# Kernel optimization log

Hardware: AMD Instinct MI355X
Metric: run time of the kernel (lower is better)

The kernel has to match this reference:

```python
import jax, jax.numpy as jnp
import numpy as np

N_NODES = 50000
N_EDGES = 800000
C = 64
N_STEPS = 4
N_MIX = 14  # sum_{i=0..3} (i+2)
NEG_SLOPE = 0.2  # PyG GATConv default negative_slope


def setup_inputs() -> dict:
    key = jax.random.key(0)
    ks = jax.random.split(key, 9)
    g = lambda k, shp: jax.random.normal(k, shp, jnp.float32) * (1.0 / np.sqrt(C))
    return {
        "x": jax.random.normal(ks[0], (N_NODES, C), jnp.float32),
        "edge_index": jax.random.randint(ks[1], (2, N_EDGES), 0, N_NODES, dtype=jnp.int64),
        "alphas": jax.random.normal(ks[2], (N_MIX, 5), jnp.float32),
        "gcn_W": g(ks[3], (N_MIX, C, C)),
        "gcn_b": jnp.zeros((N_MIX, C), jnp.float32),
        "sage_Wl": g(ks[4], (N_MIX, C, C)),
        "sage_Wr": g(ks[5], (N_MIX, C, C)),
        "sage_b": jnp.zeros((N_MIX, C), jnp.float32),
        "gat_W": g(ks[6], (N_MIX, C, C)),
        "gat_a_src": g(ks[7], (N_MIX, C)),
        "gat_a_dst": g(ks[8], (N_MIX, C)),
        "gat_b": jnp.zeros((N_MIX, C), jnp.float32),
    }


def _cell(x, edge_index, alphas, gcn_W, gcn_b, sage_Wl, sage_Wr, sage_b,
          gat_W, gat_a_src, gat_a_dst, gat_b):
    n = x.shape[0]
    src, dst = edge_index[0], edge_index[1]
    loop = jnp.arange(n)
    # edges with self-loops (used by GCN and GAT, per PyG defaults)
    src_sl = jnp.concatenate([src, loop])
    dst_sl = jnp.concatenate([dst, loop])

    # GCN symmetric normalization: deg over self-looped targets, norm per edge.
    deg = jax.ops.segment_sum(jnp.ones(src_sl.shape, jnp.float32), dst_sl, num_segments=n)
    dinv = jnp.where(deg > 0, jax.lax.rsqrt(deg), 0.0)
    gcn_norm = dinv[src_sl] * dinv[dst_sl]  # [E+N]

    # SAGE mean-aggregation denominator (no self loops; empty -> clamp to 1, sum is 0 anyway)
    cnt = jnp.maximum(
        jax.ops.segment_sum(jnp.ones(dst.shape, jnp.float32), dst, num_segments=n), 1.0)

    def gcn(h, k):
        hw = h @ gcn_W[k]  # [n, C]
        return jax.ops.segment_sum(gcn_norm[:, None] * hw[src_sl], dst_sl,
                                   num_segments=n) + gcn_b[k]

    def sage(h, k):
        agg = jax.ops.segment_sum(h[src], dst, num_segments=n) / cnt[:, None]
        return agg @ sage_Wl[k] + h @ sage_Wr[k] + sage_b[k]

    def gat(h, k):
        hw = h @ gat_W[k]  # shared lin for src/dst (same node set)
        e = (hw @ gat_a_src[k])[src_sl] + (hw @ gat_a_dst[k])[dst_sl]
        e = jnp.where(e > 0, e, NEG_SLOPE * e)  # LeakyReLU
        # segment softmax over incoming edges per target (self-loops make all segments non-empty)
        emax = jax.ops.segment_max(e, dst_sl, num_segments=n)
        ee = jnp.exp(e - emax[dst_sl])
        denom = jax.ops.segment_sum(ee, dst_sl, num_segments=n)
        a = ee / denom[dst_sl]
        return jax.ops.segment_sum(a[:, None] * hw[src_sl], dst_sl,
                                   num_segments=n) + gat_b[k]

    def mixed(h, k):
        w = jax.nn.softmax(alphas[k])  # [5]: gcn, sage, gat, identity, zero
        return w[0] * gcn(h, k) + w[1] * sage(h, k) + w[2] * gat(h, k) + w[3] * h

    states = [x, x]
    offset = 0
    for i in range(N_STEPS):
        s = 0.0
        for j in range(i + 2):
            s = s + mixed(states[j], offset + j)
        offset += i + 2
        states.append(s)
    return jnp.mean(jnp.stack(states[-N_STEPS:], axis=0), axis=0)


def reference(x, edge_index, alphas, gcn_W, gcn_b, sage_Wl, sage_Wr, sage_b,
              gat_W, gat_a_src, gat_a_dst, gat_b):
    return _cell(x, edge_index, alphas, gcn_W, gcn_b, sage_Wl, sage_Wr, sage_b,
                 gat_W, gat_a_src, gat_a_dst, gat_b)
```

## Files before the change

### kernel.cpp

```cpp
#include <hip/hip_runtime.h>

#define N_NODES 50000
#define N_EDGES 800000
#define CCH 64
#define N_MIX 14
#define NBUCK 196
#define BCAP 6144
#define ECHUNK 3125

typedef __bf16 bf16x8 __attribute__((ext_vector_type(8)));
typedef float floatx4 __attribute__((ext_vector_type(4)));

__device__ __forceinline__ float leaky(float x) {
    return fmaxf(x, 0.2f * x);
}

__global__ void prep_weights(const float* __restrict__ alphas,
                             const float* __restrict__ gcn_W, const float* __restrict__ gcn_b,
                             const float* __restrict__ sage_Wl, const float* __restrict__ sage_Wr,
                             const float* __restrict__ sage_b, const float* __restrict__ gat_Wp,
                             const float* __restrict__ a_src, const float* __restrict__ a_dst,
                             const float* __restrict__ gat_b,
                             __bf16* __restrict__ Wt, float* __restrict__ bc,
                             float* __restrict__ vs, float* __restrict__ vd) {
    int k = blockIdx.x;
    __shared__ float w[5];
    if (threadIdx.x == 0) {
        float a[5], m = -1e30f, s = 0.f;
        for (int i = 0; i < 5; ++i) { a[i] = alphas[k * 5 + i]; m = fmaxf(m, a[i]); }
        for (int i = 0; i < 5; ++i) { a[i] = __expf(a[i] - m); s += a[i]; }
        for (int i = 0; i < 5; ++i) w[i] = a[i] / s;
    }
    __syncthreads();
    float gamma = (k >= 9) ? 0.25f : 1.0f;
    float w0 = gamma * w[0], w1 = gamma * w[1], w2 = gamma * w[2], w3 = gamma * w[3];
    float idext = (k >= 11) ? 0.25f : 0.f;
    for (int idx = threadIdx.x; idx < 64 * 256; idx += blockDim.x) {
        int c = idx >> 8, j = idx & 255;
        float v;
        if (j < 64)       v = w0 * gcn_W[k * 4096 + j * 64 + c];
        else if (j < 128) v = w1 * sage_Wl[k * 4096 + (j - 64) * 64 + c];
        else if (j < 192) {
            int jj = j - 128;
            v = w1 * sage_Wr[k * 4096 + jj * 64 + c];
            if (jj == c) v += w3 + idext;
        } else {
            v = w2 * gat_Wp[k * 4096 + (j - 192) * 64 + c];
        }
        Wt[(size_t)k * 16384 + idx] = (__bf16)v;
    }
    if (threadIdx.x < 64) {
        int r = threadIdx.x;
        bc[k * 64 + r] = gamma * (w[0] * gcn_b[k * 64 + r] + w[1] * sage_b[k * 64 + r] +
                                  w[2] * gat_b[k * 64 + r]);
        float s1 = 0.f, s2 = 0.f;
        for (int j = 0; j < 64; ++j) {
            float wv_ = gat_Wp[k * 4096 + r * 64 + j];
            s1 += wv_ * a_src[k * 64 + j];
            s2 += wv_ * a_dst[k * 64 + j];
        }
        vs[k * 64 + r] = s1;
        vd[k * 64 + r] = s2;
    }
}

__global__ void prep_scoreV(const float* __restrict__ vs, const float* __restrict__ vd,
                            __bf16* __restrict__ Vph,
                            unsigned km0, unsigned km1, unsigned km2, unsigned km3,
                            unsigned nks) {
    int p = blockIdx.x;
    unsigned km = (p == 0) ? km0 : (p == 1) ? km1 : (p == 2) ? km2 : km3;
    int nk = (nks >> (p * 4)) & 15;
    for (int idx = threadIdx.x; idx < 1024; idx += blockDim.x) {
        int n = idx >> 6, kk = idx & 63;
        int t = n & 7;
        float v = 0.f;
        if (t < nk) {
            int k = (km >> (4 * t)) & 15;
            v = (n < 8) ? vs[k * 64 + kk] : vd[k * 64 + kk];
        }
        Vph[p * 1024 + n * 64 + kk] = (__bf16)v;
    }
}

__global__ void convert_bf16(const float4* __restrict__ src, __bf16* __restrict__ dst, int n4) {
    int i = blockIdx.x * blockDim.x + threadIdx.x;
    if (i < n4) {
        float4 v = src[i];
        dst[i * 4 + 0] = (__bf16)v.x;
        dst[i * 4 + 1] = (__bf16)v.y;
        dst[i * 4 + 2] = (__bf16)v.z;
        dst[i * 4 + 3] = (__bf16)v.w;
    }
}

__global__ __launch_bounds__(256) void bucket_count(const int* __restrict__ ei,
                                                    int* __restrict__ bcount) {
    __shared__ int h[NBUCK];
    for (int i = threadIdx.x; i < NBUCK; i += 256) h[i] = 0;
    __syncthreads();
    int e0 = blockIdx.x * ECHUNK;
    for (int i = threadIdx.x; i < ECHUNK; i += 256)
        atomicAdd(&h[ei[N_EDGES + e0 + i] >> 8], 1);
    __syncthreads();
    for (int i = threadIdx.x; i < NBUCK; i += 256)
        if (h[i]) atomicAdd(&bcount[i], h[i]);
}

__global__ __launch_bounds__(256) void bucket_scan(const int* __restrict__ bcount,
                                                   int* __restrict__ bbase,
                                                   int* __restrict__ row_ptr) {
    __shared__ int s[256];
    int t = threadIdx.x;
    int v = (t < NBUCK) ? bcount[t] : 0;
    s[t] = v;
    __syncthreads();
    for (int o = 1; o < 256; o <<= 1) {
        int t2 = (t >= o) ? s[t - o] : 0;
        __syncthreads();
        s[t] += t2;
        __syncthreads();
    }
    if (t < NBUCK) bbase[t + 1] = s[t];
    if (t == 0) { bbase[0] = 0; row_ptr[N_NODES] = N_EDGES; }
}

__global__ __launch_bounds__(256) void bucket_scatter(const int* __restrict__ ei,
                                                      const int* __restrict__ bbase,
                                                      int* __restrict__ bfill,
                                                      unsigned* __restrict__ pairs) {
    __shared__ int lh[NBUCK], lbase[NBUCK], lcur[NBUCK];
    int tid = threadIdx.x;
    int e0 = blockIdx.x * ECHUNK;
    for (int i = tid; i < NBUCK; i += 256) { lh[i] = 0; lcur[i] = 0; }
    __syncthreads();
    for (int i = tid; i < ECHUNK; i += 256)
        atomicAdd(&lh[ei[N_EDGES + e0 + i] >> 8], 1);
    __syncthreads();
    for (int i = tid; i < NBUCK; i += 256)
        lbase[i] = bbase[i] + ((lh[i] > 0) ? atomicAdd(&bfill[i], lh[i]) : 0);
    __syncthreads();
    for (int i = tid; i < ECHUNK; i += 256) {
        int s = ei[e0 + i];
        int d = ei[N_EDGES + e0 + i];
        int b = d >> 8;
        int pos = atomicAdd(&lcur[b], 1);
        pairs[lbase[b] + pos] = (unsigned)s | ((unsigned)(d & 255) << 16);
    }
}

__global__ __launch_bounds__(256) void bucket_sort(const unsigned* __restrict__ pairs,
                                                   const int* __restrict__ bbase,
                                                   int* __restrict__ row_ptr,
                                                   int* __restrict__ col_idx,
                                                   float* __restrict__ dinv,
                                                   float* __restrict__ cntf) {
    int b = blockIdx.x;
    __shared__ unsigned buf[BCAP];
    __shared__ int hist[256], off[256], cur[256];
    int tid = threadIdx.x;
    hist[tid] = 0;
    __syncthreads();
    int base = bbase[b], cnt = bbase[b + 1] - base;
    if (cnt > BCAP) cnt = BCAP;
    for (int i = tid; i < cnt; i += 256) {
        unsigned pr = pairs[(size_t)base + i];
        buf[i] = pr;
        atomicAdd(&hist[(pr >> 16) & 255], 1);
    }
    __syncthreads();
    int v = hist[tid];
    off[tid] = v;
    __syncthreads();
    for (int o = 1; o < 256; o <<= 1) {
        int t2 = (tid >= o) ? off[tid - o] : 0;
        __syncthreads();
        off[tid] += t2;
        __syncthreads();
    }
    int excl = off[tid] - v;
    int node = b * 256 + tid;
    if (node < N_NODES) {
        row_ptr[node] = base + excl;
        dinv[node] = rsqrtf((float)(v + 1));
        cntf[node] = (float)(v > 0 ? v : 1);
    }
    cur[tid] = excl;
    __syncthreads();
    for (int i = tid; i < cnt; i += 256) {
        unsigned pr = buf[i];
        int ln = (pr >> 16) & 255;
        int pos = atomicAdd(&cur[ln], 1);
        col_idx[base + pos] = (int)(pr & 0xffffu);
    }
}

__global__ __launch_bounds__(256) void score_mfma(const __bf16* __restrict__ hb,
                                                  const __bf16* __restrict__ V,
                                                  float* __restrict__ ssrcS,
                                                  float* __restrict__ sdstS) {
    int tid = threadIdx.x;
    int wave = tid >> 6, lane = tid & 63;
    int quad = lane >> 4, mr = lane & 15;
    int r0 = blockIdx.x * 128 + wave * 32;
    bf16x8 b0 = *(const bf16x8*)(V + mr * 64 + (quad << 3));
    bf16x8 b1 = *(const bf16x8*)(V + mr * 64 + 32 + (quad << 3));
#pragma unroll
    for (int rt = 0; rt < 2; ++rt) {
        int r = r0 + rt * 16 + mr;
        if (r > N_NODES - 1) r = N_NODES - 1;
        bf16x8 a0 = *(const bf16x8*)(hb + (size_t)r * 64 + (quad << 3));
        bf16x8 a1 = *(const bf16x8*)(hb + (size_t)r * 64 + 32 + (quad << 3));
        floatx4 acc = (floatx4){0.f, 0.f, 0.f, 0.f};
        acc = __builtin_amdgcn_mfma_f32_16x16x32_bf16(a0, b0, acc, 0, 0, 0);
        acc = __builtin_amdgcn_mfma_f32_16x16x32_bf16(a1, b1, acc, 0, 0, 0);
#pragma unroll
        for (int reg = 0; reg < 4; ++reg) {
            int row = r0 + rt * 16 + quad * 4 + reg;
            if (row < N_NODES) {
                if (mr < 8) ssrcS[(size_t)row * 8 + mr] = acc[reg];
                else        sdstS[(size_t)row * 8 + (mr - 8)] = acc[reg];
            }
        }
    }
}

template <int NK>
__global__ __launch_bounds__(128, 4) void fused_gather(
    const __bf16* __restrict__ hb, const int* __restrict__ row_ptr,
    const int* __restrict__ col_idx, const float* __restrict__ dinv,
    const float* __restrict__ cntf, const float* __restrict__ ssrcS,
    const float* __restrict__ sdstS, int soff, int doGS,
    __bf16* __restrict__ aggG, __bf16* __restrict__ aggS, __bf16* __restrict__ A) {
    int wid = blockIdx.x * 2 + (threadIdx.x >> 6);
    int lane = threadIdx.x & 63;
    int sub = lane >> 3, ln = lane & 7;
    int node = wid * 8 + sub;
    int beg = row_ptr[node], end = row_ptr[node + 1];

    float sd[NK], selfraw[NK];
    {
        float4 sv = *(const float4*)(ssrcS + (size_t)node * 8 + soff);
        float4 dvv = *(const float4*)(sdstS + (size_t)node * 8 + soff);
        float svv[4] = {sv.x, sv.y, sv.z, sv.w};
        float dvl[4] = {dvv.x, dvv.y, dvv.z, dvv.w};
#pragma unroll
        for (int t = 0; t < NK; ++t) {
            sd[t] = dvl[t];
            selfraw[t] = leaky(svv[t] + sd[t]);
        }
    }
    bf16x8 hsb = *(const bf16x8*)(hb + (size_t)node * 64 + ln * 8);
    float hs[8];
#pragma unroll
    for (int c = 0; c < 8; ++c) hs[c] = (float)hsb[c];

    float denoml[NK], acc[NK][8], accG[8], accS[8];
#pragma unroll
    for (int c = 0; c < 8; ++c) { accG[c] = 0.f; accS[c] = 0.f; }
#pragma unroll
    for (int t = 0; t < NK; ++t) {
        denoml[t] = 0.f;
#pragma unroll
        for (int c = 0; c < 8; ++c) acc[t][c] = hs[c];
    }
    for (int base = beg; base < end; base += 8) {
        int e = base + ln;
        int col = 0;
        float dv = 0.f, wv[NK];
#pragma unroll
        for (int t = 0; t < NK; ++t) wv[t] = 0.f;
        if (e < end) {
            col = col_idx[e];
            dv = dinv[col];
            float4 sv = *(const float4*)(ssrcS + (size_t)col * 8 + soff);
            float svv[4] = {sv.x, sv.y, sv.z, sv.w};
#pragma unroll
            for (int t = 0; t < NK; ++t) {
                wv[t] = __expf(leaky(svv[t] + sd[t]) - selfraw[t]);
                denoml[t] += wv[t];
            }
        }
        int jcnt = end - base;
        if (jcnt > 8) jcnt = 8;
        int cs0 = __shfl(col, (sub << 3), 64);
        bf16x8 hx = *(const bf16x8*)(hb + (size_t)cs0 * 64 + ln * 8);
        for (int j = 0; j < jcnt; ++j) {
            bf16x8 hxn;
            if (j + 1 < jcnt) {
                int csn = __shfl(col, (sub << 3) | (j + 1), 64);
                hxn = *(const bf16x8*)(hb + (size_t)csn * 64 + ln * 8);
            }
            int srcl = (sub << 3) | j;
            float dvj = __shfl(dv, srcl, 64);
            float wj[NK];
#pragma unroll
            for (int t = 0; t < NK; ++t) wj[t] = __shfl(wv[t], srcl, 64);
#pragma unroll
            for (int c = 0; c < 8; ++c) {
                float f = (float)hx[c];
                accS[c] += f;
                accG[c] += dvj * f;
#pragma unroll
                for (int t = 0; t < NK; ++t) acc[t][c] += wj[t] * f;
            }
            hx = hxn;
        }
    }
    float denom[NK];
#pragma unroll
    for (int t = 0; t < NK; ++t) {
        float w = denoml[t];
#pragma unroll
        for (int off = 1; off < 8; off <<= 1) w += __shfl_xor(w, off, 64);
        denom[t] = w + 1.0f;
    }

    if (doGS) {
        float dvn = dinv[node];
        float cin = 1.0f / cntf[node];
        bf16x8 og, os;
#pragma unroll
        for (int c = 0; c < 8; ++c) {
            os[c] = (__bf16)(accS[c] * cin);
            og[c] = (__bf16)(dvn * accG[c] + dvn * dvn * hs[c]);
        }
        *(bf16x8*)(aggS + (size_t)node * 64 + ln * 8) = os;
        *(bf16x8*)(aggG + (size_t)node * 64 + ln * 8) = og;
    }
#pragma unroll
    for (int t = 0; t < NK; ++t) {
        bf16x8 oa;
        float inv = 1.0f / denom[t];
#pragma unroll
        for (int c = 0; c < 8; ++c) oa[c] = (__bf16)(acc[t][c] * inv);
        *(bf16x8*)(A + (size_t)t * N_NODES * 64 + (size_t)node * 64 + ln * 8) = oa;
    }
}

struct GArgs {
    const __bf16* G;
    const __bf16* S;
    const __bf16* Hb;
    const __bf16* A0;
    const __bf16* Wt;
    const float* bc;
    float* tg[4];
    __bf16* shadow_ptr;
    long long slot;
    int nk;
    int initmask;
    int shadow_t;
    int kidx[8];
    int tsel[8];
};

__global__ __launch_bounds__(256) void gemm_group(GArgs a) {
    __shared__ __bf16 Wl[64 * 264];
    int tid = threadIdx.x;
    int wave = tid >> 6, lane = tid & 63;
    int quad = lane >> 4, mr = lane & 15;
    int r0 = blockIdx.x * 128 + wave * 32;
    bf16x8 gf[2][2], sf[2][2], hf[2][2];
#pragma unroll
    for (int rt = 0; rt < 2; ++rt) {
        int r = r0 + rt * 16 + mr;
        if (r > N_NODES - 1) r = N_NODES - 1;
#pragma unroll
        for (int hh = 0; hh < 2; ++hh) {
            int colj = hh * 32 + (quad << 3);
            gf[rt][hh] = *(const bf16x8*)(a.G + (size_t)r * 64 + colj);
            sf[rt][hh] = *(const bf16x8*)(a.S + (size_t)r * 64 + colj);
            hf[rt][hh] = *(const bf16x8*)(a.Hb + (size_t)r * 64 + colj);
        }
    }
    floatx4 acc[2][4];
    float bsum[4];
#pragma unroll
    for (int rt = 0; rt < 2; ++rt)
#pragma unroll
        for (int ct = 0; ct < 4; ++ct) acc[rt][ct] = (floatx4){0.f, 0.f, 0.f, 0.f};
#pragma unroll
    for (int ct = 0; ct < 4; ++ct) bsum[ct] = 0.f;
    int runstart = 0;
    for (int t = 0; t < a.nk; ++t) {
        int k = a.kidx[t];
        __syncthreads();
        {
            const uint4* src = (const uint4*)(a.Wt + (size_t)k * 16384);
            for (int i = tid; i < 2048; i += 256) {
                int row = i >> 5, colj = (i & 31) << 3;
                *(uint4*)&Wl[row * 264 + colj] = src[i];
            }
        }
        __syncthreads();
        const __bf16* Ap = a.A0 + (size_t)t * a.slot;
        bf16x8 af[2][2];
#pragma unroll
        for (int rt = 0; rt < 2; ++rt) {
            int r = r0 + rt * 16 + mr;
            if (r > N_NODES - 1) r = N_NODES - 1;
#pragma unroll
            for (int hh = 0; hh < 2; ++hh)
                af[rt][hh] = *(const bf16x8*)(Ap + (size_t)r * 64 + hh * 32 + (quad << 3));
        }
        const float* bp = a.bc + k * 64;
#pragma unroll
        for (int ct = 0; ct < 4; ++ct) bsum[ct] += bp[ct * 16 + mr];
#pragma unroll
        for (int seg = 0; seg < 4; ++seg) {
#pragma unroll
            for (int hh = 0; hh < 2; ++hh) {
                int kt = seg * 2 + hh;
                bf16x8 a0 = (seg == 0) ? gf[0][hh] : (seg == 1) ? sf[0][hh]
                            : (seg == 2) ? hf[0][hh] : af[0][hh];
                bf16x8 a1 = (seg == 0) ? gf[1][hh] : (seg == 1) ? sf[1][hh]
                            : (seg == 2) ? hf[1][hh] : af[1][hh];
#pragma unroll
                for (int ct = 0; ct < 4; ++ct) {
                    bf16x8 bfr = *(const bf16x8*)&Wl[(ct * 16 + mr) * 264 + (kt << 5) + (quad << 3)];
                    acc[0][ct] = __builtin_amdgcn_mfma_f32_16x16x32_bf16(a0, bfr, acc[0][ct], 0, 0, 0);
                    acc[1][ct] = __builtin_amdgcn_mfma_f32_16x16x32_bf16(a1, bfr, acc[1][ct], 0, 0, 0);
                }
            }
        }
        bool flush = (t == a.nk - 1) || (a.tsel[t + 1] != a.tsel[t]);
        if (flush) {
            float* tgt = a.tg[a.tsel[t]];
            int init = (a.initmask >> runstart) & 1;
            bool shadow = (t == a.shadow_t);
            __bf16* sh = a.shadow_ptr;
#pragma unroll
            for (int rt = 0; rt < 2; ++rt) {
#pragma unroll
                for (int reg = 0; reg < 4; ++reg) {
                    int r = r0 + rt * 16 + quad * 4 + reg;
                    if (r < N_NODES) {
#pragma unroll
                        for (int ct = 0; ct < 4; ++ct) {
                            int c = ct * 16 + mr;
                            float v = acc[rt][ct][reg] + bsum[ct];
                            size_t idx = (size_t)r * 64 + c;
                            float nv = init ? v : (tgt[idx] + v);
                            tgt[idx] = nv;
                            if (shadow) sh[idx] = (__bf16)nv;
                        }
                    }
                }
            }
#pragma unroll
            for (int rt = 0; rt < 2; ++rt)
#pragma unroll
                for (int ct = 0; ct < 4; ++ct) acc[rt][ct] = (floatx4){0.f, 0.f, 0.f, 0.f};
#pragma unroll
            for (int ct = 0; ct < 4; ++ct) bsum[ct] = 0.f;
            runstart = t + 1;
        }
    }
}

extern "C" void kernel_launch(void* const* d_in, const int* in_sizes, int n_in,
                              void* d_out, int out_size, void* d_ws, size_t ws_size,
                              hipStream_t stream) {
    const float* x       = (const float*)d_in[0];
    const int*   ei      = (const int*)d_in[1];
    const float* alphas  = (const float*)d_in[2];
    const float* gcn_W   = (const float*)d_in[3];
    const float* gcn_b   = (const float*)d_in[4];
    const float* sage_Wl = (const float*)d_in[5];
    const float* sage_Wr = (const float*)d_in[6];
    const float* sage_b  = (const float*)d_in[7];
    const float* gat_W   = (const float*)d_in[8];
    const float* a_src   = (const float*)d_in[9];
    const float* a_dst   = (const float*)d_in[10];
    const float* gat_b   = (const float*)d_in[11];
    float* out = (float*)d_out;

    char* p = (char*)d_ws;
    auto alloc = [&](size_t bytes) -> char* {
        char* r = p;
        p += (bytes + 255) & ~(size_t)255;
        return r;
    };
    const size_t NCf = (size_t)N_NODES * CCH;
    const size_t NC32 = NCf * 4;
    const size_t NC16 = NCf * 2;
    float* sb[3];
    sb[0] = (float*)alloc(NC32);
    sb[1] = (float*)alloc(NC32);
    sb[2] = (float*)alloc(NC32);
    __bf16* hbuf[4];
    for (int i = 0; i < 4; ++i) hbuf[i] = (__bf16*)alloc(NC16);
    __bf16* aggG = (__bf16*)alloc(NC16);
    __bf16* aggS = (__bf16*)alloc(NC16);
    float* ssrcS = (float*)alloc((size_t)N_NODES * 8 * 4);
    float* sdstS = (float*)alloc((size_t)N_NODES * 8 * 4);
    float* dinv  = (float*)alloc(N_NODES * 4);
    float* cntf  = (float*)alloc(N_NODES * 4);
    int* row_ptr = (int*)alloc((N_NODES + 1) * 4);
    int* col_idx = (int*)alloc((size_t)N_EDGES * 4);
    unsigned* pairs = (unsigned*)alloc((size_t)N_EDGES * 4);
    int* bcount  = (int*)alloc(NBUCK * 4);
    int* bfill   = (int*)alloc(NBUCK * 4);
    int* bbase   = (int*)alloc((NBUCK + 1) * 4);
    __bf16* Wt   = (__bf16*)alloc((size_t)N_MIX * 16384 * 2);
    float* bcv   = (float*)alloc(N_MIX * 64 * 4);
    float* vs    = (float*)alloc(N_MIX * 64 * 4);
    float* vd    = (float*)alloc(N_MIX * 64 * 4);
    __bf16* Vph  = (__bf16*)alloc(4 * 1024 * 2);

    size_t used = (size_t)(p - (char*)d_ws);
    int navail = (int)((ws_size > used) ? ((ws_size - used) / NC16) : 0);
    if (navail < 1) navail = 1;
    if (navail > 8) navail = 8;
    __bf16* Abuf = (__bf16*)alloc((size_t)navail * NC16);

    hipMemsetAsync(bcount, 0, NBUCK * 4, stream);
    hipMemsetAsync(bfill, 0, NBUCK * 4, stream);

    prep_weights<<<N_MIX, 256, 0, stream>>>(alphas, gcn_W, gcn_b, sage_Wl, sage_Wr, sage_b,
                                            gat_W, a_src, a_dst, gat_b, Wt, bcv, vs, vd);
    prep_scoreV<<<4, 256, 0, stream>>>(vs, vd, Vph, 0xA9653210u, 0xB74u, 0xC8u, 0xDu, 0x1238u);
    convert_bf16<<<(int)((NCf / 4 + 255) / 256), 256, 0, stream>>>((const float4*)x, hbuf[0],
                                                                   (int)(NCf / 4));
    bucket_count<<<256, 256, 0, stream>>>(ei, bcount);
    bucket_scan<<<1, 256, 0, stream>>>(bcount, bbase, row_ptr);
    bucket_scatter<<<256, 256, 0, stream>>>(ei, bbase, bfill, pairs);
    bucket_sort<<<NBUCK, 256, 0, stream>>>(pairs, bbase, row_ptr, col_idx, dinv, cntf);

    const int AGG_GRID = N_NODES / 16;
    const int GEMM_GRID = (N_NODES + 127) / 128;

    float* targ[4] = {sb[0], sb[1], sb[2], out};
    struct Phase { int nk; int ks[8]; int tg[8]; };
    const Phase ph[4] = {
        {8, {0, 1, 2, 3, 5, 6, 9, 10}, {0, 0, 1, 1, 2, 2, 3, 3}},
        {3, {4, 7, 11, 0, 0, 0, 0, 0}, {1, 2, 3, 0, 0, 0, 0, 0}},
        {2, {8, 12, 0, 0, 0, 0, 0, 0}, {2, 3, 0, 0, 0, 0, 0, 0}},
        {1, {13, 0, 0, 0, 0, 0, 0, 0}, {3, 0, 0, 0, 0, 0, 0, 0}},
    };

    auto launch_gather = [&](int nkk, const __bf16* hb, int soff, int doGS, __bf16* Aslot) {
        switch (nkk) {
            case 4: fused_gather<4><<<AGG_GRID, 128, 0, stream>>>(hb, row_ptr, col_idx, dinv, cntf, ssrcS, sdstS, soff, doGS, aggG, aggS, Aslot); break;
            case 3: fused_gather<3><<<AGG_GRID, 128, 0, stream>>>(hb, row_ptr, col_idx, dinv, cntf, ssrcS, sdstS, soff, doGS, aggG, aggS, Aslot); break;
            case 2: fused_gather<2><<<AGG_GRID, 128, 0, stream>>>(hb, row_ptr, col_idx, dinv, cntf, ssrcS, sdstS, soff, doGS, aggG, aggS, Aslot); break;
            default: fused_gather<1><<<AGG_GRID, 128, 0, stream>>>(hb, row_ptr, col_idx, dinv, cntf, ssrcS, sdstS, soff, doGS, aggG, aggS, Aslot); break;
        }
    };
    auto make_gemm = [&](const Phase& P, const __bf16* hb, int kstart, int g) {
        GArgs ga;
        ga.G = aggG; ga.S = aggS; ga.Hb = hb; ga.A0 = Abuf;
        ga.Wt = Wt; ga.bc = bcv;
        for (int i = 0; i < 4; ++i) ga.tg[i] = targ[i];
        ga.slot = (long long)NCf;
        ga.nk = g;
        ga.initmask = 0;
        ga.shadow_t = -1;
        ga.shadow_ptr = hbuf[0];
        for (int j = 0; j < g; ++j) {
            int k = P.ks[kstart + j];
            ga.kidx[j] = k;
            ga.tsel[j] = P.tg[kstart + j];
            if (k == 0 || k == 2 || k == 5 || k == 9) ga.initmask |= (1 << j);
            if (k == 1) { ga.shadow_t = j; ga.shadow_ptr = hbuf[1]; }
            if (k == 4) { ga.shadow_t = j; ga.shadow_ptr = hbuf[2]; }
            if (k == 8) { ga.shadow_t = j; ga.shadow_ptr = hbuf[3]; }
        }
        for (int j = g; j < 8; ++j) { ga.kidx[j] = 0; ga.tsel[j] = (j > 0) ? ga.tsel[j - 1] : 0; }
        gemm_group<<<GEMM_GRID, 256, 0, stream>>>(ga);
    };

    for (int st = 0; st < 4; ++st) {
        const Phase& P = ph[st];
        const __bf16* hb = hbuf[st];
        score_mfma<<<GEMM_GRID, 256, 0, stream>>>(hb, Vph + st * 1024, ssrcS, sdstS);
        if (navail >= P.nk) {
            int done = 0;
            while (done < P.nk) {
                int g = P.nk - done;
                if (g > 4) g = 4;
                launch_gather(g, hb, done, (done == 0) ? 1 : 0, Abuf + (size_t)done * NCf);
                done += g;
            }
            make_gemm(P, hb, 0, P.nk);
        } else {
            int gs = (navail < 4) ? navail : 4;
            for (int done = 0; done < P.nk;) {
                int g = gs;
                if (g > P.nk - done) g = P.nk - done;
                launch_gather(g, hb, done, (done == 0) ? 1 : 0, Abuf);
                make_gemm(P, hb, done, g);
                done += g;
            }
        }
    }
}
```

Baseline: 463.0 us.

## Degree-sort gather nodes, fuse 8-head gather, accumulate intermediate states in bf16

Adds a degree histogram, scan and scatter that build a permutation grouping nodes by in-degree, so each wave's eight nodes loop over similar edge counts and divergence drops. The fused gather now handles up to 8 attention heads in one launch, so phase 0 no longer needs two gather passes over the edges. Intermediate state buffers become bf16 (written directly into hbuf) instead of fp32 plus a bf16 shadow copy, which removes that extra traffic. The costs are more registers in the NK=8 kernel, which may lower occupancy, a few extra setup kernels, and bf16 rounding on the accumulated partial sums.

```diff
diff --git a/kernel.cpp b/kernel.cpp
--- a/kernel.cpp
+++ b/kernel.cpp
@@ -7,6 +7,7 @@
 #define NBUCK 196
 #define BCAP 6144
 #define ECHUNK 3125
+#define DBINS 64
 
 typedef __bf16 bf16x8 __attribute__((ext_vector_type(8)));
 typedef float floatx4 __attribute__((ext_vector_type(4)));
@@ -195,6 +196,56 @@
     }
 }
 
+__global__ __launch_bounds__(256) void deg_hist(const int* __restrict__ row_ptr,
+                                                int* __restrict__ dh) {
+    __shared__ int h[DBINS];
+    if (threadIdx.x < DBINS) h[threadIdx.x] = 0;
+    __syncthreads();
+    int i = blockIdx.x * 256 + threadIdx.x;
+    if (i < N_NODES) {
+        int d = row_ptr[i + 1] - row_ptr[i];
+        atomicAdd(&h[min(d, DBINS - 1)], 1);
+    }
+    __syncthreads();
+    if (threadIdx.x < DBINS && h[threadIdx.x]) atomicAdd(&dh[threadIdx.x], h[threadIdx.x]);
+}
+
+__global__ __launch_bounds__(64) void deg_scan(const int* __restrict__ dh,
+                                               int* __restrict__ dbase) {
+    int t = threadIdx.x;
+    int v = dh[t];
+    int inc = v;
+#pragma unroll
+    for (int o = 1; o < 64; o <<= 1) {
+        int t2 = __shfl_up(inc, o, 64);
+        if (t >= o) inc += t2;
+    }
+    dbase[t] = inc - v;
+}
+
+__global__ __launch_bounds__(256) void deg_scatter(const int* __restrict__ row_ptr,
+                                                   const int* __restrict__ dbase,
+                                                   int* __restrict__ dfill,
+                                                   int* __restrict__ perm) {
+    __shared__ int lh[DBINS], lbase[DBINS], lcur[DBINS];
+    int tid = threadIdx.x;
+    if (tid < DBINS) { lh[tid] = 0; lcur[tid] = 0; }
+    __syncthreads();
+    int i = blockIdx.x * 256 + tid;
+    int d = -1;
+    if (i < N_NODES) {
+        d = min(row_ptr[i + 1] - row_ptr[i], DBINS - 1);
+        atomicAdd(&lh[d], 1);
+    }
+    __syncthreads();
+    if (tid < DBINS) lbase[tid] = dbase[tid] + ((lh[tid] > 0) ? atomicAdd(&dfill[tid], lh[tid]) : 0);
+    __syncthreads();
+    if (i < N_NODES) {
+        int pos = lbase[d] + atomicAdd(&lcur[d], 1);
+        perm[pos] = i;
+    }
+}
+
 __global__ __launch_bounds__(256) void score_mfma(const __bf16* __restrict__ hb,
                                                   const __bf16* __restrict__ V,
                                                   float* __restrict__ ssrcS,
@@ -230,20 +281,28 @@
     const __bf16* __restrict__ hb, const int* __restrict__ row_ptr,
     const int* __restrict__ col_idx, const float* __restrict__ dinv,
     const float* __restrict__ cntf, const float* __restrict__ ssrcS,
-    const float* __restrict__ sdstS, int soff, int doGS,
+    const float* __restrict__ sdstS, const int* __restrict__ perm,
+    int soff, int doGS,
     __bf16* __restrict__ aggG, __bf16* __restrict__ aggS, __bf16* __restrict__ A) {
     int wid = blockIdx.x * 2 + (threadIdx.x >> 6);
     int lane = threadIdx.x & 63;
     int sub = lane >> 3, ln = lane & 7;
-    int node = wid * 8 + sub;
+    int node = perm[wid * 8 + sub];
     int beg = row_ptr[node], end = row_ptr[node + 1];
 
     float sd[NK], selfraw[NK];
     {
-        float4 sv = *(const float4*)(ssrcS + (size_t)node * 8 + soff);
-        float4 dvv = *(const float4*)(sdstS + (size_t)node * 8 + soff);
-        float svv[4] = {sv.x, sv.y, sv.z, sv.w};
-        float dvl[4] = {dvv.x, dvv.y, dvv.z, dvv.w};
+        float svv[8], dvl[8];
+        float4 a0 = *(const float4*)(ssrcS + (size_t)node * 8 + soff);
+        float4 b0 = *(const float4*)(sdstS + (size_t)node * 8 + soff);
+        svv[0] = a0.x; svv[1] = a0.y; svv[2] = a0.z; svv[3] = a0.w;
+        dvl[0] = b0.x; dvl[1] = b0.y; dvl[2] = b0.z; dvl[3] = b0.w;
+        if (NK > 4) {
+            float4 a1 = *(const float4*)(ssrcS + (size_t)node * 8 + soff + 4);
+            float4 b1 = *(const float4*)(sdstS + (size_t)node * 8 + soff + 4);
+            svv[4] = a1.x; svv[5] = a1.y; svv[6] = a1.z; svv[7] = a1.w;
+            dvl[4] = b1.x; dvl[5] = b1.y; dvl[6] = b1.z; dvl[7] = b1.w;
+        }
 #pragma unroll
         for (int t = 0; t < NK; ++t) {
             sd[t] = dvl[t];
@@ -273,8 +332,13 @@
         if (e < end) {
             col = col_idx[e];
             dv = dinv[col];
-            float4 sv = *(const float4*)(ssrcS + (size_t)col * 8 + soff);
-            float svv[4] = {sv.x, sv.y, sv.z, sv.w};
+            float svv[8];
+            float4 a0 = *(const float4*)(ssrcS + (size_t)col * 8 + soff);
+            svv[0] = a0.x; svv[1] = a0.y; svv[2] = a0.z; svv[3] = a0.w;
+            if (NK > 4) {
+                float4 a1 = *(const float4*)(ssrcS + (size_t)col * 8 + soff + 4);
+                svv[4] = a1.x; svv[5] = a1.y; svv[6] = a1.z; svv[7] = a1.w;
+            }
 #pragma unroll
             for (int t = 0; t < NK; ++t) {
                 wv[t] = __expf(leaky(svv[t] + sd[t]) - selfraw[t]);
@@ -345,12 +409,11 @@
     const __bf16* A0;
     const __bf16* Wt;
     const float* bc;
-    float* tg[4];
-    __bf16* shadow_ptr;
+    __bf16* tgb[3];
+    float* tgf;
     long long slot;
     int nk;
     int initmask;
-    int shadow_t;
     int kidx[8];
     int tsel[8];
 };
@@ -426,24 +489,43 @@
         }
         bool flush = (t == a.nk - 1) || (a.tsel[t + 1] != a.tsel[t]);
         if (flush) {
-            float* tgt = a.tg[a.tsel[t]];
+            int ts = a.tsel[t];
             int init = (a.initmask >> runstart) & 1;
-            bool shadow = (t == a.shadow_t);
-            __bf16* sh = a.shadow_ptr;
-#pragma unroll
-            for (int rt = 0; rt < 2; ++rt) {
-#pragma unroll
-                for (int reg = 0; reg < 4; ++reg) {
-                    int r = r0 + rt * 16 + quad * 4 + reg;
-                    if (r < N_NODES) {
-#pragma unroll
-                        for (int ct = 0; ct < 4; ++ct) {
-                            int c = ct * 16 + mr;
-                            float v = acc[rt][ct][reg] + bsum[ct];
-                            size_t idx = (size_t)r * 64 + c;
-                            float nv = init ? v : (tgt[idx] + v);
-                            tgt[idx] = nv;
-                            if (shadow) sh[idx] = (__bf16)nv;
+            if (ts < 3) {
+                __bf16* tgt = a.tgb[ts];
+#pragma unroll
+                for (int rt = 0; rt < 2; ++rt) {
+#pragma unroll
+                    for (int reg = 0; reg < 4; ++reg) {
+                        int r = r0 + rt * 16 + quad * 4 + reg;
+                        if (r < N_NODES) {
+#pragma unroll
+                            for (int ct = 0; ct < 4; ++ct) {
+                                int c = ct * 16 + mr;
+                                float v = acc[rt][ct][reg] + bsum[ct];
+                                size_t idx = (size_t)r * 64 + c;
+                                if (!init) v += (float)tgt[idx];
+                                tgt[idx] = (__bf16)v;
+                            }
+                        }
+                    }
+                }
+            } else {
+                float* tgt = a.tgf;
+#pragma unroll
+                for (int rt = 0; rt < 2; ++rt) {
+#pragma unroll
+                    for (int reg = 0; reg < 4; ++reg) {
+                        int r = r0 + rt * 16 + quad * 4 + reg;
+                        if (r < N_NODES) {
+#pragma unroll
+                            for (int ct = 0; ct < 4; ++ct) {
+                                int c = ct * 16 + mr;
+                                float v = acc[rt][ct][reg] + bsum[ct];
+                                size_t idx = (size_t)r * 64 + c;
+                                if (!init) v += tgt[idx];
+                                tgt[idx] = v;
+                            }
                         }
                     }
                 }
@@ -483,12 +565,7 @@
         return r;
     };
     const size_t NCf = (size_t)N_NODES * CCH;
-    const size_t NC32 = NCf * 4;
     const size_t NC16 = NCf * 2;
-    float* sb[3];
-    sb[0] = (float*)alloc(NC32);
-    sb[1] = (float*)alloc(NC32);
-    sb[2] = (float*)alloc(NC32);
     __bf16* hbuf[4];
     for (int i = 0; i < 4; ++i) hbuf[i] = (__bf16*)alloc(NC16);
     __bf16* aggG = (__bf16*)alloc(NC16);
@@ -503,6 +580,10 @@
     int* bcount  = (int*)alloc(NBUCK * 4);
     int* bfill   = (int*)alloc(NBUCK * 4);
     int* bbase   = (int*)alloc((NBUCK + 1) * 4);
+    int* dh      = (int*)alloc(DBINS * 4);
+    int* dbase   = (int*)alloc(DBINS * 4);
+    int* dfill   = (int*)alloc(DBINS * 4);
+    int* perm    = (int*)alloc(N_NODES * 4);
     __bf16* Wt   = (__bf16*)alloc((size_t)N_MIX * 16384 * 2);
     float* bcv   = (float*)alloc(N_MIX * 64 * 4);
     float* vs    = (float*)alloc(N_MIX * 64 * 4);
@@ -517,6 +598,8 @@
 
     hipMemsetAsync(bcount, 0, NBUCK * 4, stream);
     hipMemsetAsync(bfill, 0, NBUCK * 4, stream);
+    hipMemsetAsync(dh, 0, DBINS * 4, stream);
+    hipMemsetAsync(dfill, 0, DBINS * 4, stream);
 
     prep_weights<<<N_MIX, 256, 0, stream>>>(alphas, gcn_W, gcn_b, sage_Wl, sage_Wr, sage_b,
                                             gat_W, a_src, a_dst, gat_b, Wt, bcv, vs, vd);
@@ -527,11 +610,13 @@
     bucket_scan<<<1, 256, 0, stream>>>(bcount, bbase, row_ptr);
     bucket_scatter<<<256, 256, 0, stream>>>(ei, bbase, bfill, pairs);
     bucket_sort<<<NBUCK, 256, 0, stream>>>(pairs, bbase, row_ptr, col_idx, dinv, cntf);
+    deg_hist<<<NBUCK, 256, 0, stream>>>(row_ptr, dh);
+    deg_scan<<<1, 64, 0, stream>>>(dh, dbase);
+    deg_scatter<<<NBUCK, 256, 0, stream>>>(row_ptr, dbase, dfill, perm);
 
     const int AGG_GRID = N_NODES / 16;
     const int GEMM_GRID = (N_NODES + 127) / 128;
 
-    float* targ[4] = {sb[0], sb[1], sb[2], out};
     struct Phase { int nk; int ks[8]; int tg[8]; };
     const Phase ph[4] = {
         {8, {0, 1, 2, 3, 5, 6, 9, 10}, {0, 0, 1, 1, 2, 2, 3, 3}},
@@ -542,30 +627,27 @@
 
     auto launch_gather = [&](int nkk, const __bf16* hb, int soff, int doGS, __bf16* Aslot) {
         switch (nkk) {
-            case 4: fused_gather<4><<<AGG_GRID, 128, 0, stream>>>(hb, row_ptr, col_idx, dinv, cntf, ssrcS, sdstS, soff, doGS, aggG, aggS, Aslot); break;
-            case 3: fused_gather<3><<<AGG_GRID, 128, 0, stream>>>(hb, row_ptr, col_idx, dinv, cntf, ssrcS, sdstS, soff, doGS, aggG, aggS, Aslot); break;
-            case 2: fused_gather<2><<<AGG_GRID, 128, 0, stream>>>(hb, row_ptr, col_idx, dinv, cntf, ssrcS, sdstS, soff, doGS, aggG, aggS, Aslot); break;
-            default: fused_gather<1><<<AGG_GRID, 128, 0, stream>>>(hb, row_ptr, col_idx, dinv, cntf, ssrcS, sdstS, soff, doGS, aggG, aggS, Aslot); break;
+            case 8: fused_gather<8><<<AGG_GRID, 128, 0, stream>>>(hb, row_ptr, col_idx, dinv, cntf, ssrcS, sdstS, perm, soff, doGS, aggG, aggS, Aslot); break;
+            case 4: fused_gather<4><<<AGG_GRID, 128, 0, stream>>>(hb, row_ptr, col_idx, dinv, cntf, ssrcS, sdstS, perm, soff, doGS, aggG, aggS, Aslot); break;
+            case 3: fused_gather<3><<<AGG_GRID, 128, 0, stream>>>(hb, row_ptr, col_idx, dinv, cntf, ssrcS, sdstS, perm, soff, doGS, aggG, aggS, Aslot); break;
+            case 2: fused_gather<2><<<AGG_GRID, 128, 0, stream>>>(hb, row_ptr, col_idx, dinv, cntf, ssrcS, sdstS, perm, soff, doGS, aggG, aggS, Aslot); break;
+            default: fused_gather<1><<<AGG_GRID, 128, 0, stream>>>(hb, row_ptr, col_idx, dinv, cntf, ssrcS, sdstS, perm, soff, doGS, aggG, aggS, Aslot); break;
         }
     };
     auto make_gemm = [&](const Phase& P, const __bf16* hb, int kstart, int g) {
         GArgs ga;
         ga.G = aggG; ga.S = aggS; ga.Hb = hb; ga.A0 = Abuf;
         ga.Wt = Wt; ga.bc = bcv;
-        for (int i = 0; i < 4; ++i) ga.tg[i] = targ[i];
+        ga.tgb[0] = hbuf[1]; ga.tgb[1] = hbuf[2]; ga.tgb[2] = hbuf[3];
+        ga.tgf = out;
         ga.slot = (long long)NCf;
         ga.nk = g;
         ga.initmask = 0;
-        ga.shadow_t = -1;
-        ga.shadow_ptr = hbuf[0];
         for (int j = 0; j < g; ++j) {
             int k = P.ks[kstart + j];
             ga.kidx[j] = k;
             ga.tsel[j] = P.tg[kstart + j];
             if (k == 0 || k == 2 || k == 5 || k == 9) ga.initmask |= (1 << j);
-            if (k == 1) { ga.shadow_t = j; ga.shadow_ptr = hbuf[1]; }
-            if (k == 4) { ga.shadow_t = j; ga.shadow_ptr = hbuf[2]; }
-            if (k == 8) { ga.shadow_t = j; ga.shadow_ptr = hbuf[3]; }
         }
         for (int j = g; j < 8; ++j) { ga.kidx[j] = 0; ga.tsel[j] = (j > 0) ? ga.tsel[j - 1] : 0; }
         gemm_group<<<GEMM_GRID, 256, 0, stream>>>(ga);
@@ -576,13 +658,7 @@
         const __bf16* hb = hbuf[st];
         score_mfma<<<GEMM_GRID, 256, 0, stream>>>(hb, Vph + st * 1024, ssrcS, sdstS);
         if (navail >= P.nk) {
-            int done = 0;
-            while (done < P.nk) {
-                int g = P.nk - done;
-                if (g > 4) g = 4;
-                launch_gather(g, hb, done, (done == 0) ? 1 : 0, Abuf + (size_t)done * NCf);
-                done += g;
-            }
+            launch_gather(P.nk, hb, 0, 1, Abuf);
             make_gemm(P, hb, 0, P.nk);
         } else {
             int gs = (navail < 4) ? navail : 4;
```

Measured after the change: 466.2 us. About the same (+0.7%).
